# Kernel optimization log

Measured on AMD Instinct MI355X. Metric: run time of the kernel, lower is better.

Reference implementation:

```python
import jax, jax.numpy as jnp
import numpy as np

EPS = 1e-5


def _lerp_t(y, out_t):
    # trilinear interpolate with align_corners=True where only the T axis changes size
    T = y.shape[2]
    pos = jnp.arange(out_t) * ((T - 1) / (out_t - 1))
    i0 = jnp.floor(pos).astype(jnp.int32)
    i1 = jnp.minimum(i0 + 1, T - 1)
    w = (pos - i0).astype(y.dtype)[None, None, :, None, None]
    return jnp.take(y, i0, axis=2) * (1 - w) + jnp.take(y, i1, axis=2) * w


def setup_inputs() -> dict:
    key = jax.random.key(0)
    ks = jax.random.split(key, 8)
    B, C, T, H, W = 2, 32, 64, 64, 64
    N = 512
    Cf = 32   # projection_nin (backbone feature channels)
    Ch = Cf // 2
    x = jax.random.normal(ks[0], (B, C, T, H, W), jnp.float32)
    coord = jax.random.randint(ks[1], (B, N, 2), 0, H)
    # backbone stand-in: two pointwise 1x1x1 conv heads
    Wf = jax.random.normal(ks[2], (Cf, C), jnp.float32) * 0.05
    bf = jnp.zeros((Cf,), jnp.float32)
    Wr = jax.random.normal(ks[3], (1, C), jnp.float32) * 0.05
    br = jnp.zeros((1,), jnp.float32)
    # projection1: Conv1d(Cf->Ch,k=1) + BN1d(Ch) + ReLU + Conv1d(Ch->Ch,k=1)
    W1 = jax.random.normal(ks[4], (Ch, Cf), jnp.float32) * 0.1
    b1 = jnp.zeros((Ch,), jnp.float32)
    gamma = jnp.ones((Ch,), jnp.float32)
    beta = jnp.zeros((Ch,), jnp.float32)
    W2 = jax.random.normal(ks[5], (Ch, Ch), jnp.float32) * 0.1
    b2 = jnp.zeros((Ch,), jnp.float32)
    return {"x": x, "coord": coord, "Wf": Wf, "bf": bf, "Wr": Wr, "br": br,
            "W1": W1, "b1": b1, "gamma": gamma, "beta": beta, "W2": W2, "b2": b2,
            "orgt": 400, "featT": 400}


def reference(x, coord, Wf, bf, Wr, br, W1, b1, gamma, beta, W2, b2, orgt, featT):
    B, C, T, H, W = x.shape
    # backbone (pointwise conv3d heads)
    feat = jnp.einsum('oc,bcthw->bothw', Wf, x) + bf[None, :, None, None, None]
    result = jnp.einsum('oc,bcthw->bothw', Wr, x) + br[None, :, None, None, None]
    # trilinear resize along T only (H,W unchanged, align_corners=True -> identity)
    feat = _lerp_t(feat, featT)        # [B,Cf,featT,H,W]
    result = _lerp_t(result, orgt)     # [B,1,orgt,H,W]
    # presample: per-sample spatial gather at coord (h,w) pairs
    Cf = feat.shape[1]
    idx = coord[..., 0] * W + coord[..., 1]                      # [B,N]
    flat = feat.reshape(B, Cf, featT, H * W)
    g = jnp.take_along_axis(flat, idx[:, None, None, :], axis=3)  # [B,Cf,featT,N]
    g = g.reshape(B, Cf, -1)                                      # [B,Cf,featT*N]
    # projection1: pointwise conv -> BN (training stats) -> ReLU -> pointwise conv
    h = jnp.einsum('oc,bcl->bol', W1, g) + b1[None, :, None]
    mu = h.mean(axis=(0, 2), keepdims=True)
    var = ((h - mu) ** 2).mean(axis=(0, 2), keepdims=True)
    h = (h - mu) * jax.lax.rsqrt(var + EPS) * gamma[None, :, None] + beta[None, :, None]
    h = jax.nn.relu(h)
    out = jnp.einsum('oc,bcl->bol', W2, h) + b2[None, :, None]
    return out, result
```

## Files before the change

kernel.cpp:

```cpp
#include <hip/hip_runtime.h>
#include <stdint.h>

#define BB   2
#define CC   32
#define TT   64
#define HWH  4096
#define NN   512
#define CFF  32
#define CHH  16
#define TOUT 400
#define LL   (TOUT*NN)

__device__ __forceinline__ void lerp_coeff(int to, int& i0, int& i1, float& w){
  const float step = (float)(63.0 / 399.0);
  float pos = (float)to * step;
  i0 = (int)floorf(pos);
  if (i0 > TT - 1) i0 = TT - 1;
  i1 = i0 + 1; if (i1 > TT - 1) i1 = TT - 1;
  w = pos - (float)i0;
}

__global__ void k_coef(float* __restrict__ coef){
  int to = blockIdx.x * 256 + threadIdx.x;
  if (to < TOUT){
    int i0, i1; float w;
    lerp_coeff(to, i0, i1, w);
    if (i1 == i0){
      atomicAdd(coef + i0, 1.f);
      atomicAdd(coef + 64 + i0, 1.f);
    } else {
      float u = 1.f - w;
      atomicAdd(coef + i0, u);        atomicAdd(coef + 64 + i0, u * u);
      atomicAdd(coef + i1, w);        atomicAdd(coef + 64 + i1, w * w);
      atomicAdd(coef + 128 + i0, 2.f * w * u);
    }
  }
}

__global__ __launch_bounds__(256) void k_r(const float* __restrict__ x, const float* __restrict__ Wr,
                                           const float* __restrict__ br, float* __restrict__ r){
  int tid = blockIdx.x * 256 + threadIdx.x;
  int hw0 = (tid & 1023) << 2;
  int t   = (tid >> 10) & 63;
  int b   = tid >> 16;
  float br0 = br[0];
  float4 acc = make_float4(br0, br0, br0, br0);
  const float* xp = x + ((size_t)(b * CC) * TT + t) * HWH + hw0;
  #pragma unroll
  for (int c = 0; c < CC; ++c){
    float4 v = *reinterpret_cast<const float4*>(xp + (size_t)c * TT * HWH);
    float w = Wr[c];
    acc.x += w * v.x;  acc.y += w * v.y;  acc.z += w * v.z;  acc.w += w * v.w;
  }
  *reinterpret_cast<float4*>(r + ((size_t)(b * TT + t)) * HWH + hw0) = acc;
}

__global__ __launch_bounds__(256) void k_result(const float* __restrict__ r, float* __restrict__ outR){
  int tid = blockIdx.x * 256 + threadIdx.x;
  int hw0  = (tid & 1023) << 2;
  int rest = tid >> 10;
  int b  = rest >= TOUT ? 1 : 0;
  int to = rest - b * TOUT;
  int i0, i1; float w;
  lerp_coeff(to, i0, i1, w);
  float4 a = *reinterpret_cast<const float4*>(r + ((size_t)(b * TT + i0)) * HWH + hw0);
  float4 c = *reinterpret_cast<const float4*>(r + ((size_t)(b * TT + i1)) * HWH + hw0);
  float4 o;
  o.x = a.x + w * (c.x - a.x);
  o.y = a.y + w * (c.y - a.y);
  o.z = a.z + w * (c.z - a.z);
  o.w = a.w + w * (c.w - a.w);
  *reinterpret_cast<float4*>(outR + ((size_t)(b * TOUT + to)) * HWH + hw0) = o;
}

__global__ __launch_bounds__(256) void k_gather(const float* __restrict__ x, const int* __restrict__ coord,
                                                const float* __restrict__ Wf, const float* __restrict__ bfv,
                                                float* __restrict__ G){
  __shared__ float sWfT[CC][CFF];
  __shared__ float sbf[CFF];
  for (int i = threadIdx.x; i < CFF * CC; i += 256){
    int cf = i >> 5, c = i & 31;
    sWfT[c][cf] = Wf[i];
  }
  if (threadIdx.x < CFF) sbf[threadIdx.x] = bfv[threadIdx.x];
  __syncthreads();
  int lane = threadIdx.x & 63;
  int sub  = threadIdx.x & 3;
  int e = blockIdx.x * 64 + ((int)threadIdx.x >> 2);
  int n = e & 511, t = (e >> 9) & 63, b = e >> 15;
  int h  = coord[(b * NN + n) * 2 + 0];
  int wq = coord[(b * NN + n) * 2 + 1];
  int hw = h * 64 + wq;
  const float* xp = x + (((size_t)(b * CC + sub * 8)) * TT + t) * HWH + hw;
  float xv[8];
  #pragma unroll
  for (int j = 0; j < 8; ++j) xv[j] = xp[(size_t)j * (TT * HWH)];
  float acc[8];
  #pragma unroll
  for (int i = 0; i < 8; ++i) acc[i] = sbf[sub * 8 + i];
  int grp = lane & ~3;
  #pragma unroll
  for (int j = 0; j < 8; ++j){
    #pragma unroll
    for (int src = 0; src < 4; ++src){
      float xc = __shfl(xv[j], grp + src, 64);
      int c = src * 8 + j;
      const float4 wa = *reinterpret_cast<const float4*>(&sWfT[c][sub * 8]);
      const float4 wb = *reinterpret_cast<const float4*>(&sWfT[c][sub * 8 + 4]);
      acc[0] += wa.x * xc;  acc[1] += wa.y * xc;  acc[2] += wa.z * xc;  acc[3] += wa.w * xc;
      acc[4] += wb.x * xc;  acc[5] += wb.y * xc;  acc[6] += wb.z * xc;  acc[7] += wb.w * xc;
    }
  }
  float* Gp = G + ((size_t)((b * TT + t) * NN + n)) * CFF + sub * 8;
  *reinterpret_cast<float4*>(Gp)     = make_float4(acc[0], acc[1], acc[2], acc[3]);
  *reinterpret_cast<float4*>(Gp + 4) = make_float4(acc[4], acc[5], acc[6], acc[7]);
}

__global__ __launch_bounds__(256) void k_mom(const float* __restrict__ G, const float* __restrict__ W1,
                                             const float* __restrict__ coef, float* __restrict__ stats){
  __shared__ float sW1[CHH][CFF];
  __shared__ float sco[192];
  __shared__ float red[4][32];
  for (int i = threadIdx.x; i < CHH * CFF; i += 256) sW1[i >> 5][i & 31] = W1[i];
  if (threadIdx.x < 192) sco[threadIdx.x] = coef[threadIdx.x];
  __syncthreads();
  int t = threadIdx.x & 63;
  int e = blockIdx.x * 4 + ((int)threadIdx.x >> 6);
  int b = e >> 9, n = e & 511;
  const float* gp = G + ((size_t)((b * TT + t) * NN + n)) * CFF;
  float g[CFF];
  #pragma unroll
  for (int c = 0; c < CFF; c += 4){
    float4 v = *reinterpret_cast<const float4*>(gp + c);
    g[c] = v.x; g[c+1] = v.y; g[c+2] = v.z; g[c+3] = v.w;
  }
  float qt = sco[t], at = sco[64 + t], ct = sco[128 + t];
  float v1[CHH], v2[CHH];
  #pragma unroll
  for (int o = 0; o < CHH; ++o){
    float y = 0.f;
    #pragma unroll
    for (int c = 0; c < CFF; ++c) y += sW1[o][c] * g[c];
    float yn = __shfl_down(y, 1, 64);
    v1[o] = qt * y;
    v2[o] = at * y * y + ct * y * yn;
  }
  #pragma unroll
  for (int o = 0; o < CHH; ++o){
    #pragma unroll
    for (int s = 32; s > 0; s >>= 1){
      v1[o] += __shfl_down(v1[o], s, 64);
      v2[o] += __shfl_down(v2[o], s, 64);
    }
  }
  int wave = threadIdx.x >> 6, lane = threadIdx.x & 63;
  if (lane == 0){
    #pragma unroll
    for (int o = 0; o < CHH; ++o){ red[wave][o] = v1[o]; red[wave][16 + o] = v2[o]; }
  }
  __syncthreads();
  if (threadIdx.x < 32){
    float v = red[0][threadIdx.x] + red[1][threadIdx.x] + red[2][threadIdx.x] + red[3][threadIdx.x];
    atomicAdd(stats + threadIdx.x, v);
  }
}

__global__ void k_fin(const float* __restrict__ gamma, const float* __restrict__ beta,
                      const float* __restrict__ b1, float* __restrict__ stats){
  int o = threadIdx.x;
  if (o < CHH){
    const float L2f = (float)(BB * (long long)LL);
    float inv = 1.0f / L2f;
    float A1 = stats[o], A2 = stats[16 + o], bb = b1[o];
    float mu  = (A1 + L2f * bb) * inv;
    float ex2 = (A2 + 2.f * bb * A1 + L2f * bb * bb) * inv;
    float var = ex2 - mu * mu;
    float sc  = gamma[o] * (1.0f / sqrtf(var + 1e-5f));
    stats[32 + o] = sc;
    stats[48 + o] = beta[o] - mu * sc;
  }
}

__global__ __launch_bounds__(256) void k_out(const float* __restrict__ G, const float* __restrict__ W1,
                                             const float* __restrict__ b1, const float* __restrict__ W2,
                                             const float* __restrict__ b2, const float* __restrict__ stats,
                                             float* __restrict__ out){
  __shared__ float sW1[CHH][CFF];
  __shared__ float sW2[CHH][CHH];
  __shared__ float sb1[CHH], sb2[CHH], ssc[CHH], ssh[CHH];
  for (int i = threadIdx.x; i < CHH * CFF; i += 256) sW1[i >> 5][i & 31] = W1[i];
  for (int i = threadIdx.x; i < CHH * CHH; i += 256) sW2[i >> 4][i & 15] = W2[i];
  if (threadIdx.x < CHH){
    sb1[threadIdx.x] = b1[threadIdx.x];
    sb2[threadIdx.x] = b2[threadIdx.x];
    ssc[threadIdx.x] = stats[32 + threadIdx.x];
    ssh[threadIdx.x] = stats[48 + threadIdx.x];
  }
  __syncthreads();
  int xcd = blockIdx.x & 7, loc = blockIdx.x >> 3;
  int eb = xcd * 200 + loc;
  int li  = eb * 256 + (int)threadIdx.x;
  int b   = li / LL;
  int rem = li - b * LL;
  int to  = rem >> 9;
  int n   = rem & 511;
  int i0, i1; float w;
  lerp_coeff(to, i0, i1, w);
  const float* g0 = G + ((size_t)((b * TT + i0) * NN + n)) * CFF;
  const float* g1 = G + ((size_t)((b * TT + i1) * NN + n)) * CFF;
  float g[CFF];
  #pragma unroll
  for (int c = 0; c < CFF; c += 4){
    float4 a = *reinterpret_cast<const float4*>(g0 + c);
    float4 d = *reinterpret_cast<const float4*>(g1 + c);
    g[c]   = a.x + w * (d.x - a.x);
    g[c+1] = a.y + w * (d.y - a.y);
    g[c+2] = a.z + w * (d.z - a.z);
    g[c+3] = a.w + w * (d.w - a.w);
  }
  float hr[CHH];
  #pragma unroll
  for (int o = 0; o < CHH; ++o){
    float h = sb1[o];
    #pragma unroll
    for (int c = 0; c < CFF; ++c) h += sW1[o][c] * g[c];
    hr[o] = fmaxf(h * ssc[o] + ssh[o], 0.0f);
  }
  #pragma unroll
  for (int o2 = 0; o2 < CHH; ++o2){
    float v = sb2[o2];
    #pragma unroll
    for (int o = 0; o < CHH; ++o) v += sW2[o2][o] * hr[o];
    out[((size_t)(b * CHH + o2)) * LL + rem] = v;
  }
}

extern "C" void kernel_launch(void* const* d_in, const int* in_sizes, int n_in,
                              void* d_out, int out_size, void* d_ws, size_t ws_size,
                              hipStream_t stream){
  (void)in_sizes; (void)n_in; (void)out_size; (void)ws_size;
  const float* x     = (const float*)d_in[0];
  const int*   coord = (const int*)d_in[1];
  const float* Wf    = (const float*)d_in[2];
  const float* bfv   = (const float*)d_in[3];
  const float* Wr    = (const float*)d_in[4];
  const float* br    = (const float*)d_in[5];
  const float* W1    = (const float*)d_in[6];
  const float* b1    = (const float*)d_in[7];
  const float* gamma = (const float*)d_in[8];
  const float* beta  = (const float*)d_in[9];
  const float* W2    = (const float*)d_in[10];
  const float* b2    = (const float*)d_in[11];

  float* ws    = (float*)d_ws;
  float* r     = ws;
  float* G     = ws + 524288;
  float* stats = ws + 524288 + 2097152;
  float* coefp = stats + 64;

  float* out  = (float*)d_out;
  float* outR = out + (size_t)BB * CHH * LL;

  hipMemsetAsync(stats, 0, 256 * sizeof(float), stream);
  k_coef  <<<2,    256, 0, stream>>>(coefp);
  k_r     <<<512,  256, 0, stream>>>(x, Wr, br, r);
  k_gather<<<1024, 256, 0, stream>>>(x, coord, Wf, bfv, G);
  k_result<<<3200, 256, 0, stream>>>(r, outR);
  k_mom   <<<256,  256, 0, stream>>>(G, W1, coefp, stats);
  k_fin   <<<1,    64,  0, stream>>>(gamma, beta, b1, stats);
  k_out   <<<1600, 256, 0, stream>>>(G, W1, b1, W2, b2, stats, out);
}
```

Baseline: 203.9 us.

## Fold W1 into backbone projection and drop auxiliary kernels

Precomposes W1·Wf and W1·bf so the gather kernel directly produces the 16-channel pre-BN activation Z instead of the 32-channel feature G. This halves the intermediate buffer and removes the per-element 32x16 matvec from both the moment and output kernels. The lerp coefficient computation moves into shared memory inside k_mom, stats zeroing moves into k_r, and BN finalization moves into k_out, eliminating a memset and two tiny launches. Each k_z block redundantly recomputes the small composed matrix.

```diff
diff --git a/kernel.cpp b/kernel.cpp
--- a/kernel.cpp
+++ b/kernel.cpp
@@ -20,25 +20,10 @@
   w = pos - (float)i0;
 }
 
-__global__ void k_coef(float* __restrict__ coef){
-  int to = blockIdx.x * 256 + threadIdx.x;
-  if (to < TOUT){
-    int i0, i1; float w;
-    lerp_coeff(to, i0, i1, w);
-    if (i1 == i0){
-      atomicAdd(coef + i0, 1.f);
-      atomicAdd(coef + 64 + i0, 1.f);
-    } else {
-      float u = 1.f - w;
-      atomicAdd(coef + i0, u);        atomicAdd(coef + 64 + i0, u * u);
-      atomicAdd(coef + i1, w);        atomicAdd(coef + 64 + i1, w * w);
-      atomicAdd(coef + 128 + i0, 2.f * w * u);
-    }
-  }
-}
-
 __global__ __launch_bounds__(256) void k_r(const float* __restrict__ x, const float* __restrict__ Wr,
-                                           const float* __restrict__ br, float* __restrict__ r){
+                                           const float* __restrict__ br, float* __restrict__ r,
+                                           float* __restrict__ stats){
+  if (blockIdx.x == 0 && threadIdx.x < 32) stats[threadIdx.x] = 0.f;
   int tid = blockIdx.x * 256 + threadIdx.x;
   int hw0 = (tid & 1023) << 2;
   int t   = (tid >> 10) & 63;
@@ -73,16 +58,25 @@
   *reinterpret_cast<float4*>(outR + ((size_t)(b * TOUT + to)) * HWH + hw0) = o;
 }
 
-__global__ __launch_bounds__(256) void k_gather(const float* __restrict__ x, const int* __restrict__ coord,
-                                                const float* __restrict__ Wf, const float* __restrict__ bfv,
-                                                float* __restrict__ G){
-  __shared__ float sWfT[CC][CFF];
-  __shared__ float sbf[CFF];
-  for (int i = threadIdx.x; i < CFF * CC; i += 256){
-    int cf = i >> 5, c = i & 31;
-    sWfT[c][cf] = Wf[i];
-  }
-  if (threadIdx.x < CFF) sbf[threadIdx.x] = bfv[threadIdx.x];
+__global__ __launch_bounds__(256) void k_z(const float* __restrict__ x, const int* __restrict__ coord,
+                                           const float* __restrict__ Wf, const float* __restrict__ bfv,
+                                           const float* __restrict__ W1, const float* __restrict__ b1,
+                                           float* __restrict__ Z){
+  __shared__ float sWT[CC][CHH];
+  __shared__ float scz[CHH];
+  for (int i = threadIdx.x; i < CHH * CC; i += 256){
+    int o = i >> 5, c = i & 31;
+    float v = 0.f;
+    #pragma unroll
+    for (int k = 0; k < CFF; ++k) v += W1[o * CFF + k] * Wf[k * CC + c];
+    sWT[c][o] = v;
+  }
+  if (threadIdx.x < CHH){
+    float v = b1[threadIdx.x];
+    #pragma unroll
+    for (int k = 0; k < CFF; ++k) v += W1[threadIdx.x * CFF + k] * bfv[k];
+    scz[threadIdx.x] = v;
+  }
   __syncthreads();
   int lane = threadIdx.x & 63;
   int sub  = threadIdx.x & 3;
@@ -95,9 +89,7 @@
   float xv[8];
   #pragma unroll
   for (int j = 0; j < 8; ++j) xv[j] = xp[(size_t)j * (TT * HWH)];
-  float acc[8];
-  #pragma unroll
-  for (int i = 0; i < 8; ++i) acc[i] = sbf[sub * 8 + i];
+  float acc0 = scz[sub * 4], acc1 = scz[sub * 4 + 1], acc2 = scz[sub * 4 + 2], acc3 = scz[sub * 4 + 3];
   int grp = lane & ~3;
   #pragma unroll
   for (int j = 0; j < 8; ++j){
@@ -105,45 +97,49 @@
     for (int src = 0; src < 4; ++src){
       float xc = __shfl(xv[j], grp + src, 64);
       int c = src * 8 + j;
-      const float4 wa = *reinterpret_cast<const float4*>(&sWfT[c][sub * 8]);
-      const float4 wb = *reinterpret_cast<const float4*>(&sWfT[c][sub * 8 + 4]);
-      acc[0] += wa.x * xc;  acc[1] += wa.y * xc;  acc[2] += wa.z * xc;  acc[3] += wa.w * xc;
-      acc[4] += wb.x * xc;  acc[5] += wb.y * xc;  acc[6] += wb.z * xc;  acc[7] += wb.w * xc;
+      const float4 w4 = *reinterpret_cast<const float4*>(&sWT[c][sub * 4]);
+      acc0 += w4.x * xc;  acc1 += w4.y * xc;  acc2 += w4.z * xc;  acc3 += w4.w * xc;
     }
   }
-  float* Gp = G + ((size_t)((b * TT + t) * NN + n)) * CFF + sub * 8;
-  *reinterpret_cast<float4*>(Gp)     = make_float4(acc[0], acc[1], acc[2], acc[3]);
-  *reinterpret_cast<float4*>(Gp + 4) = make_float4(acc[4], acc[5], acc[6], acc[7]);
-}
-
-__global__ __launch_bounds__(256) void k_mom(const float* __restrict__ G, const float* __restrict__ W1,
-                                             const float* __restrict__ coef, float* __restrict__ stats){
-  __shared__ float sW1[CHH][CFF];
+  *reinterpret_cast<float4*>(Z + ((size_t)((b * TT + t) * NN + n)) * CHH + sub * 4)
+      = make_float4(acc0, acc1, acc2, acc3);
+}
+
+__global__ __launch_bounds__(256) void k_mom(const float* __restrict__ Z, float* __restrict__ stats){
   __shared__ float sco[192];
   __shared__ float red[4][32];
-  for (int i = threadIdx.x; i < CHH * CFF; i += 256) sW1[i >> 5][i & 31] = W1[i];
-  if (threadIdx.x < 192) sco[threadIdx.x] = coef[threadIdx.x];
+  if (threadIdx.x < 192) sco[threadIdx.x] = 0.f;
+  __syncthreads();
+  for (int to = threadIdx.x; to < TOUT; to += 256){
+    int i0, i1; float w;
+    lerp_coeff(to, i0, i1, w);
+    if (i1 == i0){
+      atomicAdd(&sco[i0], 1.f);  atomicAdd(&sco[64 + i0], 1.f);
+    } else {
+      float u = 1.f - w;
+      atomicAdd(&sco[i0], u);        atomicAdd(&sco[64 + i0], u * u);
+      atomicAdd(&sco[i1], w);        atomicAdd(&sco[64 + i1], w * w);
+      atomicAdd(&sco[128 + i0], 2.f * w * u);
+    }
+  }
   __syncthreads();
   int t = threadIdx.x & 63;
   int e = blockIdx.x * 4 + ((int)threadIdx.x >> 6);
   int b = e >> 9, n = e & 511;
-  const float* gp = G + ((size_t)((b * TT + t) * NN + n)) * CFF;
-  float g[CFF];
-  #pragma unroll
-  for (int c = 0; c < CFF; c += 4){
-    float4 v = *reinterpret_cast<const float4*>(gp + c);
-    g[c] = v.x; g[c+1] = v.y; g[c+2] = v.z; g[c+3] = v.w;
+  const float* zp = Z + ((size_t)((b * TT + t) * NN + n)) * CHH;
+  float z[CHH];
+  #pragma unroll
+  for (int c = 0; c < CHH; c += 4){
+    float4 v = *reinterpret_cast<const float4*>(zp + c);
+    z[c] = v.x; z[c+1] = v.y; z[c+2] = v.z; z[c+3] = v.w;
   }
   float qt = sco[t], at = sco[64 + t], ct = sco[128 + t];
   float v1[CHH], v2[CHH];
   #pragma unroll
   for (int o = 0; o < CHH; ++o){
-    float y = 0.f;
-    #pragma unroll
-    for (int c = 0; c < CFF; ++c) y += sW1[o][c] * g[c];
-    float yn = __shfl_down(y, 1, 64);
-    v1[o] = qt * y;
-    v2[o] = at * y * y + ct * y * yn;
+    float zn = __shfl_down(z[o], 1, 64);
+    v1[o] = qt * z[o];
+    v2[o] = at * z[o] * z[o] + ct * z[o] * zn;
   }
   #pragma unroll
   for (int o = 0; o < CHH; ++o){
@@ -165,36 +161,22 @@
   }
 }
 
-__global__ void k_fin(const float* __restrict__ gamma, const float* __restrict__ beta,
-                      const float* __restrict__ b1, float* __restrict__ stats){
-  int o = threadIdx.x;
-  if (o < CHH){
-    const float L2f = (float)(BB * (long long)LL);
-    float inv = 1.0f / L2f;
-    float A1 = stats[o], A2 = stats[16 + o], bb = b1[o];
-    float mu  = (A1 + L2f * bb) * inv;
-    float ex2 = (A2 + 2.f * bb * A1 + L2f * bb * bb) * inv;
-    float var = ex2 - mu * mu;
-    float sc  = gamma[o] * (1.0f / sqrtf(var + 1e-5f));
-    stats[32 + o] = sc;
-    stats[48 + o] = beta[o] - mu * sc;
-  }
-}
-
-__global__ __launch_bounds__(256) void k_out(const float* __restrict__ G, const float* __restrict__ W1,
-                                             const float* __restrict__ b1, const float* __restrict__ W2,
-                                             const float* __restrict__ b2, const float* __restrict__ stats,
+__global__ __launch_bounds__(256) void k_out(const float* __restrict__ Z, const float* __restrict__ W2,
+                                             const float* __restrict__ b2, const float* __restrict__ gamma,
+                                             const float* __restrict__ beta, const float* __restrict__ stats,
                                              float* __restrict__ out){
-  __shared__ float sW1[CHH][CFF];
   __shared__ float sW2[CHH][CHH];
-  __shared__ float sb1[CHH], sb2[CHH], ssc[CHH], ssh[CHH];
-  for (int i = threadIdx.x; i < CHH * CFF; i += 256) sW1[i >> 5][i & 31] = W1[i];
+  __shared__ float sb2[CHH], ssc[CHH], ssh[CHH];
   for (int i = threadIdx.x; i < CHH * CHH; i += 256) sW2[i >> 4][i & 15] = W2[i];
   if (threadIdx.x < CHH){
-    sb1[threadIdx.x] = b1[threadIdx.x];
-    sb2[threadIdx.x] = b2[threadIdx.x];
-    ssc[threadIdx.x] = stats[32 + threadIdx.x];
-    ssh[threadIdx.x] = stats[48 + threadIdx.x];
+    int o = threadIdx.x;
+    const float inv = 1.0f / (float)(BB * (long long)LL);
+    float mu  = stats[o] * inv;
+    float var = stats[16 + o] * inv - mu * mu;
+    float sc  = gamma[o] * (1.0f / sqrtf(var + 1e-5f));
+    ssc[o] = sc;
+    ssh[o] = beta[o] - mu * sc;
+    sb2[o] = b2[o];
   }
   __syncthreads();
   int xcd = blockIdx.x & 7, loc = blockIdx.x >> 3;
@@ -206,25 +188,21 @@
   int n   = rem & 511;
   int i0, i1; float w;
   lerp_coeff(to, i0, i1, w);
-  const float* g0 = G + ((size_t)((b * TT + i0) * NN + n)) * CFF;
-  const float* g1 = G + ((size_t)((b * TT + i1) * NN + n)) * CFF;
-  float g[CFF];
-  #pragma unroll
-  for (int c = 0; c < CFF; c += 4){
-    float4 a = *reinterpret_cast<const float4*>(g0 + c);
-    float4 d = *reinterpret_cast<const float4*>(g1 + c);
-    g[c]   = a.x + w * (d.x - a.x);
-    g[c+1] = a.y + w * (d.y - a.y);
-    g[c+2] = a.z + w * (d.z - a.z);
-    g[c+3] = a.w + w * (d.w - a.w);
-  }
+  const float* z0 = Z + ((size_t)((b * TT + i0) * NN + n)) * CHH;
+  const float* z1 = Z + ((size_t)((b * TT + i1) * NN + n)) * CHH;
   float hr[CHH];
   #pragma unroll
-  for (int o = 0; o < CHH; ++o){
-    float h = sb1[o];
-    #pragma unroll
-    for (int c = 0; c < CFF; ++c) h += sW1[o][c] * g[c];
-    hr[o] = fmaxf(h * ssc[o] + ssh[o], 0.0f);
+  for (int c = 0; c < CHH; c += 4){
+    float4 a = *reinterpret_cast<const float4*>(z0 + c);
+    float4 d = *reinterpret_cast<const float4*>(z1 + c);
+    float h0 = a.x + w * (d.x - a.x);
+    float h1 = a.y + w * (d.y - a.y);
+    float h2 = a.z + w * (d.z - a.z);
+    float h3 = a.w + w * (d.w - a.w);
+    hr[c]   = fmaxf(h0 * ssc[c]   + ssh[c],   0.0f);
+    hr[c+1] = fmaxf(h1 * ssc[c+1] + ssh[c+1], 0.0f);
+    hr[c+2] = fmaxf(h2 * ssc[c+2] + ssh[c+2], 0.0f);
+    hr[c+3] = fmaxf(h3 * ssc[c+3] + ssh[c+3], 0.0f);
   }
   #pragma unroll
   for (int o2 = 0; o2 < CHH; ++o2){
@@ -254,19 +232,15 @@
 
   float* ws    = (float*)d_ws;
   float* r     = ws;
-  float* G     = ws + 524288;
-  float* stats = ws + 524288 + 2097152;
-  float* coefp = stats + 64;
+  float* Z     = ws + 524288;
+  float* stats = ws + 524288 + 1048576;
 
   float* out  = (float*)d_out;
   float* outR = out + (size_t)BB * CHH * LL;
 
-  hipMemsetAsync(stats, 0, 256 * sizeof(float), stream);
-  k_coef  <<<2,    256, 0, stream>>>(coefp);
-  k_r     <<<512,  256, 0, stream>>>(x, Wr, br, r);
-  k_gather<<<1024, 256, 0, stream>>>(x, coord, Wf, bfv, G);
+  k_r     <<<512,  256, 0, stream>>>(x, Wr, br, r, stats);
+  k_z     <<<1024, 256, 0, stream>>>(x, coord, Wf, bfv, W1, b1, Z);
   k_result<<<3200, 256, 0, stream>>>(r, outR);
-  k_mom   <<<256,  256, 0, stream>>>(G, W1, coefp, stats);
-  k_fin   <<<1,    64,  0, stream>>>(gamma, beta, b1, stats);
-  k_out   <<<1600, 256, 0, stream>>>(G, W1, b1, W2, b2, stats, out);
-}
+  k_mom   <<<256,  256, 0, stream>>>(Z, stats);
+  k_out   <<<1600, 256, 0, stream>>>(Z, W2, b2, gamma, beta, stats, out);
+}
```

Result: faster. 179.5 us (-12.0%).
